# Kernel optimization log

Hardware: AMD Instinct MI355X
Metric: run time of the kernel (lower is better)

## Reference

```python
import jax, jax.numpy as jnp
import numpy as np

N, E = 50000, 800000
IN_DIM = 128
OUT_DIM = 128
H = 8
D = OUT_DIM // H  # head_dim = 16
LN_EPS = 1e-5


def setup_inputs() -> dict:
    key = jax.random.key(0)
    ks = jax.random.split(key, 16)
    s_in = 1.0 / np.sqrt(IN_DIM)
    s_out = 1.0 / np.sqrt(OUT_DIM)
    return {
        "x": jax.random.normal(ks[0], (N, IN_DIM), dtype=jnp.float32),
        "edge_index": jax.random.randint(ks[1], (2, E), 0, N, dtype=jnp.int32),
        "edge_attr": jax.random.uniform(ks[2], (E,), dtype=jnp.float32),
        # per-head TransformerConv params, stacked over heads (heads=1 per conv)
        "Wq": jax.random.normal(ks[3], (H, IN_DIM, D), dtype=jnp.float32) * s_in,
        "bq": jnp.zeros((H, D), dtype=jnp.float32),
        "Wk": jax.random.normal(ks[4], (H, IN_DIM, D), dtype=jnp.float32) * s_in,
        "bk": jnp.zeros((H, D), dtype=jnp.float32),
        "Wv": jax.random.normal(ks[5], (H, IN_DIM, D), dtype=jnp.float32) * s_in,
        "bv": jnp.zeros((H, D), dtype=jnp.float32),
        "We": jax.random.normal(ks[6], (H, D), dtype=jnp.float32),  # lin_edge (edge_dim=1, no bias)
        "Wskip": jax.random.normal(ks[7], (H, IN_DIM, D), dtype=jnp.float32) * s_in,
        "bskip": jnp.zeros((H, D), dtype=jnp.float32),
        "Wo": jax.random.normal(ks[8], (OUT_DIM, OUT_DIM), dtype=jnp.float32) * s_out,
        "bo": jnp.zeros((OUT_DIM,), dtype=jnp.float32),
        "gamma": jnp.ones((OUT_DIM,), dtype=jnp.float32),
        "beta": jnp.zeros((OUT_DIM,), dtype=jnp.float32),
    }


def reference(x, edge_index, edge_attr, Wq, bq, Wk, bk, Wv, bv, We, Wskip, bskip, Wo, bo, gamma, beta):
    n = x.shape[0]
    h, _, d = Wq.shape
    src, dst = edge_index[0], edge_index[1]
    # node-level projections for all heads at once: [N, H, D]
    q = jnp.einsum('ni,hid->nhd', x, Wq) + bq
    k = jnp.einsum('ni,hid->nhd', x, Wk) + bk
    v = jnp.einsum('ni,hid->nhd', x, Wv) + bv
    # edge embedding: lin_edge on scalar edge_attr -> [E, H, D]
    e = edge_attr[:, None, None] * We[None, :, :]
    # attention logits per edge/head: q_dst . (k_src + e) / sqrt(d)
    ke = k[src] + e
    alpha = jnp.einsum('ehd,ehd->eh', q[dst], ke) / jnp.sqrt(jnp.asarray(d, x.dtype))
    # segment softmax over destination nodes
    m = jax.ops.segment_max(alpha, dst, num_segments=n)  # [N, H]
    m = jnp.where(jnp.isfinite(m), m, 0.0)
    ex = jnp.exp(alpha - m[dst])
    denom = jax.ops.segment_sum(ex, dst, num_segments=n)
    w = ex / jnp.maximum(denom[dst], 1e-16)  # [E, H]
    # weighted aggregation of (v_src + e)
    agg = jax.ops.segment_sum(w[:, :, None] * (v[src] + e), dst, num_segments=n)  # [N, H, D]
    # root/skip connection inside each TransformerConv
    skip = jnp.einsum('ni,hid->nhd', x, Wskip) + bskip
    heads_cat = (agg + skip).reshape(n, h * d)  # concat over heads -> [N, OUT_DIM]
    out = heads_cat @ Wo + bo
    out = out + x  # residual (in_dim == out_dim)
    mu = out.mean(-1, keepdims=True)
    var = out.var(-1, keepdims=True)
    out = (out - mu) * jax.lax.rsqrt(var + LN_EPS) * gamma + beta
    return out
```

## Files before the change

### kernel.cpp

```cpp
#include <hip/hip_runtime.h>
#include <stdint.h>
#include <math.h>

#define IN_DIM 128
#define H_HEADS 8
#define HD 16

typedef __attribute__((ext_vector_type(8))) short bf16x8;
typedef __attribute__((ext_vector_type(4))) float f32x4;

__device__ __forceinline__ unsigned short f2bf_rne(float f) {
    unsigned int u = __float_as_uint(f);
    unsigned int r = (u + 0x7fffu + ((u >> 16) & 1u)) >> 16;
    return (unsigned short)r;
}
__device__ __forceinline__ float bf2f(unsigned short h) {
    return __uint_as_float(((unsigned int)h) << 16);
}

__device__ __forceinline__ void split_f8(const float4 f0, const float4 f1,
                                         bf16x8& h8, bf16x8& l8) {
    float ff[8] = {f0.x, f0.y, f0.z, f0.w, f1.x, f1.y, f1.z, f1.w};
    union { bf16x8 v; unsigned short u[8]; } H, L;
#pragma unroll
    for (int j = 0; j < 8; ++j) {
        H.u[j] = f2bf_rne(ff[j]);
        L.u[j] = f2bf_rne(ff[j] - bf2f(H.u[j]));
    }
    h8 = H.v; l8 = L.v;
}

__device__ __forceinline__ void stage_B(const unsigned short* __restrict__ src,
                                        unsigned short* __restrict__ lds, int t)
{
#pragma unroll
    for (int j = 0; j < 8; ++j) {
        int idx16 = t + j * 256;
        int c = idx16 >> 4, kcol = idx16 & 15;
        uint4 v = *reinterpret_cast<const uint4*>(src + (size_t)c * 128 + kcol * 8);
        *reinterpret_cast<uint4*>(lds + c * 128 + ((kcol ^ (c & 15)) * 8)) = v;
    }
}
__device__ __forceinline__ bf16x8 read_B(const unsigned short* __restrict__ lds,
                                         int c, int kcol)
{
    return *reinterpret_cast<const bf16x8*>(lds + c * 128 + ((kcol ^ (c & 15)) * 8));
}

__global__ __launch_bounds__(256)
void prep_count_kernel(const float* __restrict__ Wq, const float* __restrict__ Wk,
                       const float* __restrict__ Wv, const float* __restrict__ Wsk,
                       const float* __restrict__ Wo,
                       const float* __restrict__ bq, const float* __restrict__ bk,
                       const float* __restrict__ bv, const float* __restrict__ bsk,
                       unsigned short* __restrict__ WtH, unsigned short* __restrict__ WtL,
                       float* __restrict__ bias_cat,
                       const int* __restrict__ ei, int* __restrict__ deg, int E)
{
    const int b = blockIdx.x;
    const int t = threadIdx.x;
    if (b >= 5) {
        int e = (b - 5) * 256 + t;
        if (e < E) atomicAdd(&deg[ei[E + e]], 1);
        return;
    }
    const int p = b;
    const float* src = (p == 0) ? Wq : (p == 1) ? Wk : (p == 2) ? Wv : (p == 3) ? Wsk : Wo;
    unsigned short* dh = WtH + (size_t)p * 16384;
    unsigned short* dl = WtL + (size_t)p * 16384;
#pragma unroll
    for (int j = 0; j < 64; ++j) {
        int o = t + j * 256;
        int c = o >> 7, k = o & 127;
        float v;
        if (p < 4) {
            int h = c >> 4, d = c & 15;
            v = src[(size_t)h * 2048 + (size_t)k * 16 + d];
        } else {
            v = src[(size_t)k * 128 + c];
        }
        unsigned short hi = f2bf_rne(v);
        unsigned short lo = f2bf_rne(v - bf2f(hi));
        dh[o] = hi; dl[o] = lo;
    }
    if (p < 4 && t < 128) {
        const float* bb = (p == 0) ? bq : (p == 1) ? bk : (p == 2) ? bv : bsk;
        bias_cat[p * 128 + t] = bb[t];
    }
}

__global__ __launch_bounds__(256)
void gemm_proj_kernel(const float* __restrict__ A,
                      const unsigned short* __restrict__ WtH_base,
                      const unsigned short* __restrict__ WtL_base,
                      const float* __restrict__ bias_cat,
                      float* __restrict__ qout, float* __restrict__ skipout,
                      unsigned short* __restrict__ kvout, int N)
{
    __shared__ unsigned short Bs[16384];
    const int t = threadIdx.x;
    const int lane = t & 63;
    const int w = t >> 6;
    const int lr = lane & 15;
    const int lk = lane >> 4;
    const int p = blockIdx.y;
    const int brow0 = blockIdx.x * 64 + w * 16;
    const int arow = min(brow0 + lr, N - 1);
    const float* ap = A + (size_t)arow * 128;

    bf16x8 ah[4], al[4];
#pragma unroll
    for (int ks = 0; ks < 4; ++ks) {
        float4 f0 = *reinterpret_cast<const float4*>(ap + ks * 32 + lk * 8);
        float4 f1 = *reinterpret_cast<const float4*>(ap + ks * 32 + lk * 8 + 4);
        split_f8(f0, f1, ah[ks], al[ks]);
    }

    f32x4 acc[8];
#pragma unroll
    for (int ni = 0; ni < 8; ++ni) acc[ni] = (f32x4){0.f, 0.f, 0.f, 0.f};

    stage_B(WtH_base + (size_t)p * 16384, Bs, t);
    __syncthreads();
#pragma unroll
    for (int ks = 0; ks < 4; ++ks)
#pragma unroll
        for (int ni = 0; ni < 8; ++ni) {
            bf16x8 bh = read_B(Bs, ni * 16 + lr, ks * 4 + lk);
            acc[ni] = __builtin_amdgcn_mfma_f32_16x16x32_bf16(ah[ks], bh, acc[ni], 0, 0, 0);
            acc[ni] = __builtin_amdgcn_mfma_f32_16x16x32_bf16(al[ks], bh, acc[ni], 0, 0, 0);
        }
    __syncthreads();
    stage_B(WtL_base + (size_t)p * 16384, Bs, t);
    __syncthreads();
#pragma unroll
    for (int ks = 0; ks < 4; ++ks)
#pragma unroll
        for (int ni = 0; ni < 8; ++ni) {
            bf16x8 bl = read_B(Bs, ni * 16 + lr, ks * 4 + lk);
            acc[ni] = __builtin_amdgcn_mfma_f32_16x16x32_bf16(ah[ks], bl, acc[ni], 0, 0, 0);
        }

    const float* bias = bias_cat + p * 128;
    if (p == 0 || p == 3) {
        float* outp = (p == 0) ? qout : skipout;
#pragma unroll
        for (int ni = 0; ni < 8; ++ni) {
            int col = ni * 16 + lr;
            float bc = bias[col];
#pragma unroll
            for (int r = 0; r < 4; ++r) {
                int gr = brow0 + lk * 4 + r;
                if (gr < N) outp[(size_t)gr * 128 + col] = acc[ni][r] + bc;
            }
        }
    } else {
        unsigned int* kvu = (unsigned int*)kvout;
        const int slot = (p == 1) ? 0 : 1;
#pragma unroll
        for (int ni = 0; ni < 8; ++ni) {
            int col = ni * 16 + lr;
            float bc = bias[col];
#pragma unroll
            for (int r = 0; r < 4; ++r) {
                unsigned int s = f2bf_rne(acc[ni][r] + bc);
                unsigned int o = __shfl_xor((int)s, 1);
                int gr = brow0 + lk * 4 + r;
                if (((lr & 1) == 0) && gr < N)
                    kvu[(size_t)gr * 128 + 2 * (col >> 1) + slot] = s | (o << 16);
            }
        }
    }
}

__global__ __launch_bounds__(256)
void gemm_out_ln_kernel(const float* __restrict__ A,
                        const unsigned short* __restrict__ BtH_t,
                        const unsigned short* __restrict__ BtL_t,
                        const float* __restrict__ bo,
                        const float* __restrict__ res,
                        const float* __restrict__ gamma,
                        const float* __restrict__ beta,
                        float* __restrict__ out, int N)
{
    __shared__ unsigned short Bs[16384];
    __shared__ float lnS[2][32], lnSq[2][32];
    const int t = threadIdx.x;
    const int lane = t & 63;
    const int w = t >> 6;
    const int lr = lane & 15;
    const int lk = lane >> 4;
    const int ch = w & 1;
    const int rg = w >> 1;
    const int brow0 = blockIdx.x * 32 + rg * 16;
    const int arow = min(brow0 + lr, N - 1);
    const float* ap = A + (size_t)arow * 128;

    bf16x8 ah[4], al[4];
#pragma unroll
    for (int ks = 0; ks < 4; ++ks) {
        float4 f0 = *reinterpret_cast<const float4*>(ap + ks * 32 + lk * 8);
        float4 f1 = *reinterpret_cast<const float4*>(ap + ks * 32 + lk * 8 + 4);
        split_f8(f0, f1, ah[ks], al[ks]);
    }

    f32x4 acc[4];
#pragma unroll
    for (int ni = 0; ni < 4; ++ni) acc[ni] = (f32x4){0.f, 0.f, 0.f, 0.f};

    stage_B(BtH_t, Bs, t);
    __syncthreads();
#pragma unroll
    for (int ks = 0; ks < 4; ++ks)
#pragma unroll
        for (int ni = 0; ni < 4; ++ni) {
            bf16x8 bh = read_B(Bs, ch * 64 + ni * 16 + lr, ks * 4 + lk);
            acc[ni] = __builtin_amdgcn_mfma_f32_16x16x32_bf16(ah[ks], bh, acc[ni], 0, 0, 0);
            acc[ni] = __builtin_amdgcn_mfma_f32_16x16x32_bf16(al[ks], bh, acc[ni], 0, 0, 0);
        }
    __syncthreads();
    stage_B(BtL_t, Bs, t);
    __syncthreads();
#pragma unroll
    for (int ks = 0; ks < 4; ++ks)
#pragma unroll
        for (int ni = 0; ni < 4; ++ni) {
            bf16x8 bl = read_B(Bs, ch * 64 + ni * 16 + lr, ks * 4 + lk);
            acc[ni] = __builtin_amdgcn_mfma_f32_16x16x32_bf16(ah[ks], bl, acc[ni], 0, 0, 0);
        }

#pragma unroll
    for (int ni = 0; ni < 4; ++ni) {
        int col = ch * 64 + ni * 16 + lr;
        float bc = bo[col];
#pragma unroll
        for (int r = 0; r < 4; ++r) {
            int gr = brow0 + lk * 4 + r;
            float rv = (gr < N) ? res[(size_t)gr * 128 + col] : 0.f;
            acc[ni][r] += bc + rv;
        }
    }
    float ps[4], pq[4];
#pragma unroll
    for (int r = 0; r < 4; ++r) {
        float s = 0.f, sq = 0.f;
#pragma unroll
        for (int ni = 0; ni < 4; ++ni) { float v = acc[ni][r]; s += v; sq += v * v; }
#pragma unroll
        for (int mk = 1; mk < 16; mk <<= 1) {
            s  += __shfl_xor(s, mk);
            sq += __shfl_xor(sq, mk);
        }
        ps[r] = s; pq[r] = sq;
    }
    if (lr == 0) {
#pragma unroll
        for (int r = 0; r < 4; ++r) {
            lnS [ch][rg * 16 + lk * 4 + r] = ps[r];
            lnSq[ch][rg * 16 + lk * 4 + r] = pq[r];
        }
    }
    __syncthreads();
#pragma unroll
    for (int r = 0; r < 4; ++r) {
        int rib = rg * 16 + lk * 4 + r;
        float s  = lnS [0][rib] + lnS [1][rib];
        float sq = lnSq[0][rib] + lnSq[1][rib];
        float mean = s * (1.0f / 128.0f);
        float var  = sq * (1.0f / 128.0f) - mean * mean;
        float inv  = rsqrtf(var + 1e-5f);
        int gr = brow0 + lk * 4 + r;
        if (gr < N) {
#pragma unroll
            for (int ni = 0; ni < 4; ++ni) {
                int col = ch * 64 + ni * 16 + lr;
                out[(size_t)gr * 128 + col] =
                    (acc[ni][r] - mean) * inv * gamma[col] + beta[col];
            }
        }
    }
}

__global__ __launch_bounds__(1024)
void scan_kernel(const int* __restrict__ deg, int* __restrict__ offs,
                 int* __restrict__ cursor, int N)
{
    __shared__ int wsum[16];
    __shared__ int chunk_total_s;
    const int t = threadIdx.x;
    const int lane = t & 63, wid = t >> 6;
    int running = 0;
    for (int base = 0; base < N; base += 4096) {
        int v[4];
        int idx = base + t * 4;
#pragma unroll
        for (int j = 0; j < 4; ++j) { int i = idx + j; v[j] = (i < N) ? deg[i] : 0; }
        int ls = v[0] + v[1] + v[2] + v[3];
        int inc = ls;
#pragma unroll
        for (int off = 1; off < 64; off <<= 1) {
            int y = __shfl_up(inc, off);
            if (lane >= off) inc += y;
        }
        if (lane == 63) wsum[wid] = inc;
        __syncthreads();
        if (t < 16) {
            int winc = wsum[t];
            for (int off = 1; off < 16; off <<= 1) {
                int y = __shfl_up(winc, off);
                if (t >= off) winc += y;
            }
            wsum[t] = winc;
            if (t == 15) chunk_total_s = winc;
        }
        __syncthreads();
        int wexcl = (wid == 0) ? 0 : wsum[wid - 1];
        int texcl = running + wexcl + (inc - ls);
        int pre = 0;
#pragma unroll
        for (int j = 0; j < 4; ++j) {
            int i = idx + j;
            if (i < N) { offs[i] = texcl + pre; cursor[i] = texcl + pre; }
            pre += v[j];
        }
        running += chunk_total_s;
        __syncthreads();
    }
    if (t == 0) offs[N] = running;
}

__global__ void scatter_kernel(const int* __restrict__ ei, const float* __restrict__ ea,
                               int* __restrict__ cursor, int2* __restrict__ csr, int E)
{
    int e = blockIdx.x * 256 + threadIdx.x;
    if (e < E) {
        int s = ei[e], d = ei[E + e];
        int pos = atomicAdd(&cursor[d], 1);
        csr[pos] = make_int2(s, __float_as_int(ea[e]));
    }
}

#define GATHER(ec) (*reinterpret_cast<const ushort4*>(kvb + (size_t)(ec).x * 256 + 4 * lane))
#define PROCESS(ec, g, m, s, a0, a1) do { \
    float eav_ = __int_as_float((ec).y); \
    float ew0_ = eav_ * we2.x, ew1_ = eav_ * we2.y; \
    float dot_ = q2.x * (bf2f((g).x) + ew0_) + q2.y * (bf2f((g).y) + ew1_); \
    dot_ += __shfl_xor(dot_, 1); \
    dot_ += __shfl_xor(dot_, 2); \
    dot_ += __shfl_xor(dot_, 4); \
    float alpha_ = dot_ * 0.25f; \
    float d_ = alpha_ - (m); \
    float e_ = __expf(-fabsf(d_)); \
    bool up_ = d_ > 0.f; \
    float pv_ = up_ ? 1.f : e_; \
    float sc_ = up_ ? e_ : 1.f; \
    (m) = up_ ? alpha_ : (m); \
    (s) = (s) * sc_ + pv_; \
    (a0) = (a0) * sc_ + pv_ * (bf2f((g).z) + ew0_); \
    (a1) = (a1) * sc_ + pv_ * (bf2f((g).w) + ew1_); \
} while (0)

__global__ __launch_bounds__(256)
void agg_kernel(const float* __restrict__ qb, const float* __restrict__ sb,
                const unsigned short* __restrict__ kvb,
                const int* __restrict__ offs, const int2* __restrict__ csr,
                const float* __restrict__ We, float* __restrict__ heads_cat, int N)
{
    const int lane = threadIdx.x & 63;
    const int node = blockIdx.x * 4 + (threadIdx.x >> 6);
    if (node >= N) return;

    const float2 q2  = *reinterpret_cast<const float2*>(qb + (size_t)node * 128 + 2 * lane);
    const float2 we2 = *reinterpret_cast<const float2*>(We + 2 * lane);

    const int e0 = offs[node];
    const int cnt = offs[node + 1] - e0;

    float mA = -__builtin_huge_valf(), sA = 0.f, a0A = 0.f, a1A = 0.f;
    float mB = -__builtin_huge_valf(), sB = 0.f, a0B = 0.f, a1B = 0.f;

    int2 c0, c1, c2, c3, c4, c5;
    ushort4 g0, g1, g2, g3;
    if (cnt > 0) c0 = csr[e0];
    if (cnt > 1) c1 = csr[e0 + 1];
    if (cnt > 2) c2 = csr[e0 + 2];
    if (cnt > 3) c3 = csr[e0 + 3];
    if (cnt > 4) c4 = csr[e0 + 4];
    if (cnt > 5) c5 = csr[e0 + 5];
    if (cnt > 0) g0 = GATHER(c0);
    if (cnt > 1) g1 = GATHER(c1);
    if (cnt > 2) g2 = GATHER(c2);
    if (cnt > 3) g3 = GATHER(c3);

    int i = 0;
    for (; i + 1 < cnt; i += 2) {
        PROCESS(c0, g0, mA, sA, a0A, a1A);
        PROCESS(c1, g1, mB, sB, a0B, a1B);
        c0 = c2; c1 = c3; g0 = g2; g1 = g3;
        c2 = c4; c3 = c5;
        if (i + 6 < cnt) c4 = csr[e0 + i + 6];
        if (i + 7 < cnt) c5 = csr[e0 + i + 7];
        if (i + 4 < cnt) g2 = GATHER(c2);
        if (i + 5 < cnt) g3 = GATHER(c3);
    }
    if (i < cnt) PROCESS(c0, g0, mA, sA, a0A, a1A);

    float s, a0, a1;
    {
        float nm = fmaxf(mA, mB);
        float eA = (cnt > 0) ? __expf(mA - nm) : 0.f;
        float eB = (cnt > 1) ? __expf(mB - nm) : 0.f;
        s  = sA * eA + sB * eB;
        a0 = a0A * eA + a0B * eB;
        a1 = a1A * eA + a1B * eB;
    }

    float inv = 1.0f / fmaxf(s, 1e-16f);
    const float2 sk = *reinterpret_cast<const float2*>(sb + (size_t)node * 128 + 2 * lane);
    float2 o;
    o.x = a0 * inv + sk.x;
    o.y = a1 * inv + sk.y;
    *reinterpret_cast<float2*>(heads_cat + (size_t)node * 128 + 2 * lane) = o;
}

extern "C" void kernel_launch(void* const* d_in, const int* in_sizes, int n_in,
                              void* d_out, int out_size, void* d_ws, size_t ws_size,
                              hipStream_t stream)
{
    const float* x    = (const float*)d_in[0];
    const int*   ei   = (const int*)d_in[1];
    const float* ea   = (const float*)d_in[2];
    const float* Wq   = (const float*)d_in[3];
    const float* bq   = (const float*)d_in[4];
    const float* Wk   = (const float*)d_in[5];
    const float* bk   = (const float*)d_in[6];
    const float* Wv   = (const float*)d_in[7];
    const float* bv   = (const float*)d_in[8];
    const float* We   = (const float*)d_in[9];
    const float* Wsk  = (const float*)d_in[10];
    const float* bsk  = (const float*)d_in[11];
    const float* Wo   = (const float*)d_in[12];
    const float* bo   = (const float*)d_in[13];
    const float* gamma= (const float*)d_in[14];
    const float* beta = (const float*)d_in[15];
    const int N = in_sizes[0] / 128;
    const int E = in_sizes[1] / 2;
    float* out = (float*)d_out;

    char* w = (char*)d_ws;
    float* qarr      = (float*)w; w += (size_t)N * 128 * sizeof(float);
    float* skiparr   = (float*)w; w += (size_t)N * 128 * sizeof(float);
    unsigned short* kv = (unsigned short*)w; w += (size_t)N * 256 * sizeof(unsigned short);
    float* heads_cat = (float*)w; w += (size_t)N * 128 * sizeof(float);
    int*   deg       = (int*)w;   w += ((size_t)N + 16) * sizeof(int);
    int*   offs      = (int*)w;   w += ((size_t)N + 16) * sizeof(int);
    int*   cursor    = (int*)w;   w += ((size_t)N + 16) * sizeof(int);
    int2*  csr       = (int2*)w;  w += (size_t)E * sizeof(int2);
    unsigned short* WtH = (unsigned short*)w; w += (size_t)5 * 16384 * sizeof(unsigned short);
    unsigned short* WtL = (unsigned short*)w; w += (size_t)5 * 16384 * sizeof(unsigned short);
    float* bias_cat  = (float*)w; w += 4 * 128 * sizeof(float);

    hipMemsetAsync(deg, 0, (size_t)N * sizeof(int), stream);

    const int cntBlocks = (E + 255) / 256;
    prep_count_kernel<<<5 + cntBlocks, 256, 0, stream>>>(Wq, Wk, Wv, Wsk, Wo, bq, bk, bv, bsk,
                                                         WtH, WtL, bias_cat, ei, deg, E);

    dim3 gProj((N + 63) / 64, 4);
    gemm_proj_kernel<<<gProj, 256, 0, stream>>>(x, WtH, WtL, bias_cat, qarr, skiparr, kv, N);

    scan_kernel<<<1, 1024, 0, stream>>>(deg, offs, cursor, N);
    scatter_kernel<<<(E + 255) / 256, 256, 0, stream>>>(ei, ea, cursor, csr, E);
    agg_kernel<<<(N + 3) / 4, 256, 0, stream>>>(qarr, skiparr, kv, offs, csr, We, heads_cat, N);

    gemm_out_ln_kernel<<<(N + 31) / 32, 256, 0, stream>>>(heads_cat,
                                                          WtH + (size_t)4 * 16384,
                                                          WtL + (size_t)4 * 16384,
                                                          bo, x, gamma, beta, out, N);
}
```

Measured before the change: 376.5 us.

## Split each node's edges across two half-waves with 16-byte KV gathers

The aggregation kernel now has each half of a 64-lane wave handle alternate edges of a node. Each lane covers 4 channels with a single 16-byte load of interleaved K/V bf16, and the two partial online-softmax states are merged with cross-half shuffles. The edge-embedding term in the logit is precomputed once per node as q·We, so each edge needs fewer shuffle steps and multiplies. The bf16 conversion helper is also swapped for the HIP intrinsic. The aim is more independent gathers in flight and fewer per-edge reductions, at the cost of more registers and an extra merge step per node.

Measured after the change: 357.0 us. 1.05x faster.

```diff
diff --git a/kernel.cpp b/kernel.cpp
--- a/kernel.cpp
+++ b/kernel.cpp
@@ -1,4 +1,5 @@
 #include <hip/hip_runtime.h>
+#include <hip/hip_bf16.h>
 #include <stdint.h>
 #include <math.h>
 
@@ -9,10 +10,9 @@
 typedef __attribute__((ext_vector_type(8))) short bf16x8;
 typedef __attribute__((ext_vector_type(4))) float f32x4;
 
-__device__ __forceinline__ unsigned short f2bf_rne(float f) {
-    unsigned int u = __float_as_uint(f);
-    unsigned int r = (u + 0x7fffu + ((u >> 16) & 1u)) >> 16;
-    return (unsigned short)r;
+__device__ __forceinline__ unsigned short f2bf(float f) {
+    __hip_bfloat16 h = __float2bfloat16(f);
+    return reinterpret_cast<unsigned short&>(h);
 }
 __device__ __forceinline__ float bf2f(unsigned short h) {
     return __uint_as_float(((unsigned int)h) << 16);
@@ -24,8 +24,8 @@
     union { bf16x8 v; unsigned short u[8]; } H, L;
 #pragma unroll
     for (int j = 0; j < 8; ++j) {
-        H.u[j] = f2bf_rne(ff[j]);
-        L.u[j] = f2bf_rne(ff[j] - bf2f(H.u[j]));
+        H.u[j] = f2bf(ff[j]);
+        L.u[j] = f2bf(ff[j] - bf2f(H.u[j]));
     }
     h8 = H.v; l8 = L.v;
 }
@@ -79,8 +79,8 @@
         } else {
             v = src[(size_t)k * 128 + c];
         }
-        unsigned short hi = f2bf_rne(v);
-        unsigned short lo = f2bf_rne(v - bf2f(hi));
+        unsigned short hi = f2bf(v);
+        unsigned short lo = f2bf(v - bf2f(hi));
         dh[o] = hi; dl[o] = lo;
     }
     if (p < 4 && t < 128) {
@@ -163,7 +163,7 @@
             float bc = bias[col];
 #pragma unroll
             for (int r = 0; r < 4; ++r) {
-                unsigned int s = f2bf_rne(acc[ni][r] + bc);
+                unsigned int s = f2bf(acc[ni][r] + bc);
                 unsigned int o = __shfl_xor((int)s, 1);
                 int gr = brow0 + lk * 4 + r;
                 if (((lr & 1) == 0) && gr < N)
@@ -340,26 +340,6 @@
     }
 }
 
-#define GATHER(ec) (*reinterpret_cast<const ushort4*>(kvb + (size_t)(ec).x * 256 + 4 * lane))
-#define PROCESS(ec, g, m, s, a0, a1) do { \
-    float eav_ = __int_as_float((ec).y); \
-    float ew0_ = eav_ * we2.x, ew1_ = eav_ * we2.y; \
-    float dot_ = q2.x * (bf2f((g).x) + ew0_) + q2.y * (bf2f((g).y) + ew1_); \
-    dot_ += __shfl_xor(dot_, 1); \
-    dot_ += __shfl_xor(dot_, 2); \
-    dot_ += __shfl_xor(dot_, 4); \
-    float alpha_ = dot_ * 0.25f; \
-    float d_ = alpha_ - (m); \
-    float e_ = __expf(-fabsf(d_)); \
-    bool up_ = d_ > 0.f; \
-    float pv_ = up_ ? 1.f : e_; \
-    float sc_ = up_ ? e_ : 1.f; \
-    (m) = up_ ? alpha_ : (m); \
-    (s) = (s) * sc_ + pv_; \
-    (a0) = (a0) * sc_ + pv_ * (bf2f((g).z) + ew0_); \
-    (a1) = (a1) * sc_ + pv_ * (bf2f((g).w) + ew1_); \
-} while (0)
-
 __global__ __launch_bounds__(256)
 void agg_kernel(const float* __restrict__ qb, const float* __restrict__ sb,
                 const unsigned short* __restrict__ kvb,
@@ -369,58 +349,94 @@
     const int lane = threadIdx.x & 63;
     const int node = blockIdx.x * 4 + (threadIdx.x >> 6);
     if (node >= N) return;
-
-    const float2 q2  = *reinterpret_cast<const float2*>(qb + (size_t)node * 128 + 2 * lane);
-    const float2 we2 = *reinterpret_cast<const float2*>(We + 2 * lane);
+    const int h32 = lane & 31;
+    const int half = lane >> 5;
+
+    const float4 q4  = *reinterpret_cast<const float4*>(qb + (size_t)node * 128 + 4 * h32);
+    const float4 we4 = *reinterpret_cast<const float4*>(We + 4 * h32);
+
+    float qwe = q4.x * we4.x + q4.y * we4.y + q4.z * we4.z + q4.w * we4.w;
+    qwe += __shfl_xor(qwe, 1);
+    qwe += __shfl_xor(qwe, 2);
 
     const int e0 = offs[node];
     const int cnt = offs[node + 1] - e0;
-
-    float mA = -__builtin_huge_valf(), sA = 0.f, a0A = 0.f, a1A = 0.f;
-    float mB = -__builtin_huge_valf(), sB = 0.f, a0B = 0.f, a1B = 0.f;
-
-    int2 c0, c1, c2, c3, c4, c5;
-    ushort4 g0, g1, g2, g3;
-    if (cnt > 0) c0 = csr[e0];
-    if (cnt > 1) c1 = csr[e0 + 1];
-    if (cnt > 2) c2 = csr[e0 + 2];
-    if (cnt > 3) c3 = csr[e0 + 3];
-    if (cnt > 4) c4 = csr[e0 + 4];
-    if (cnt > 5) c5 = csr[e0 + 5];
-    if (cnt > 0) g0 = GATHER(c0);
-    if (cnt > 1) g1 = GATHER(c1);
-    if (cnt > 2) g2 = GATHER(c2);
-    if (cnt > 3) g3 = GATHER(c3);
-
-    int i = 0;
-    for (; i + 1 < cnt; i += 2) {
-        PROCESS(c0, g0, mA, sA, a0A, a1A);
-        PROCESS(c1, g1, mB, sB, a0B, a1B);
-        c0 = c2; c1 = c3; g0 = g2; g1 = g3;
-        c2 = c4; c3 = c5;
-        if (i + 6 < cnt) c4 = csr[e0 + i + 6];
-        if (i + 7 < cnt) c5 = csr[e0 + i + 7];
-        if (i + 4 < cnt) g2 = GATHER(c2);
-        if (i + 5 < cnt) g3 = GATHER(c3);
-    }
-    if (i < cnt) PROCESS(c0, g0, mA, sA, a0A, a1A);
-
-    float s, a0, a1;
-    {
-        float nm = fmaxf(mA, mB);
-        float eA = (cnt > 0) ? __expf(mA - nm) : 0.f;
-        float eB = (cnt > 1) ? __expf(mB - nm) : 0.f;
-        s  = sA * eA + sB * eB;
-        a0 = a0A * eA + a0B * eB;
-        a1 = a1A * eA + a1B * eB;
-    }
-
-    float inv = 1.0f / fmaxf(s, 1e-16f);
-    const float2 sk = *reinterpret_cast<const float2*>(sb + (size_t)node * 128 + 2 * lane);
-    float2 o;
-    o.x = a0 * inv + sk.x;
-    o.y = a1 * inv + sk.y;
-    *reinterpret_cast<float2*>(heads_cat + (size_t)node * 128 + 2 * lane) = o;
+    const int myCnt = (cnt > half) ? ((cnt - half + 1) >> 1) : 0;
+    const int2* cp = csr + e0 + half;
+
+    float m = -__builtin_huge_valf();
+    float s = 0.f, a0 = 0.f, a1 = 0.f, a2 = 0.f, a3 = 0.f;
+
+#define KVG(ec) (*reinterpret_cast<const uint4*>(kvb + (size_t)(ec).x * 256 + 8 * h32))
+#define PROC(ec, u) do { \
+    float eav_ = __int_as_float((ec).y); \
+    float k0_ = __uint_as_float((u).x << 16); \
+    float k1_ = __uint_as_float((u).x & 0xffff0000u); \
+    float k2_ = __uint_as_float((u).z << 16); \
+    float k3_ = __uint_as_float((u).z & 0xffff0000u); \
+    float part_ = q4.x * k0_ + q4.y * k1_ + q4.z * k2_ + q4.w * k3_; \
+    part_ += __shfl_xor(part_, 1); \
+    part_ += __shfl_xor(part_, 2); \
+    float alpha_ = (part_ + eav_ * qwe) * 0.25f; \
+    float d_ = alpha_ - m; \
+    float e_ = __expf(-fabsf(d_)); \
+    bool up_ = d_ > 0.f; \
+    float pv_ = up_ ? 1.f : e_; \
+    float sc_ = up_ ? e_ : 1.f; \
+    m = up_ ? alpha_ : m; \
+    float t_ = pv_ * eav_; \
+    float v0_ = __uint_as_float((u).y << 16); \
+    float v1_ = __uint_as_float((u).y & 0xffff0000u); \
+    float v2_ = __uint_as_float((u).w << 16); \
+    float v3_ = __uint_as_float((u).w & 0xffff0000u); \
+    s  = fmaf(s,  sc_, pv_); \
+    a0 = fmaf(a0, sc_, fmaf(t_, we4.x, pv_ * v0_)); \
+    a1 = fmaf(a1, sc_, fmaf(t_, we4.y, pv_ * v1_)); \
+    a2 = fmaf(a2, sc_, fmaf(t_, we4.z, pv_ * v2_)); \
+    a3 = fmaf(a3, sc_, fmaf(t_, we4.w, pv_ * v3_)); \
+} while (0)
+
+    int2 c0v, c1v, cnv;
+    uint4 g0v, g1v;
+    if (myCnt > 0) c0v = cp[0];
+    if (myCnt > 1) c1v = cp[2];
+    if (myCnt > 0) g0v = KVG(c0v);
+    if (myCnt > 1) g1v = KVG(c1v);
+
+    for (int j = 0; j < myCnt; ++j) {
+        if (j + 2 < myCnt) cnv = cp[2 * j + 4];
+        PROC(c0v, g0v);
+        c0v = c1v; g0v = g1v; c1v = cnv;
+        if (j + 2 < myCnt) g1v = KVG(c1v);
+    }
+
+    float om = __shfl_xor(m, 32);
+    float os = __shfl_xor(s, 32);
+    float o0 = __shfl_xor(a0, 32);
+    float o1 = __shfl_xor(a1, 32);
+    float o2 = __shfl_xor(a2, 32);
+    float o3 = __shfl_xor(a3, 32);
+    float nm = fmaxf(m, om);
+    float eS = (s  > 0.f) ? __expf(m  - nm) : 0.f;
+    float eO = (os > 0.f) ? __expf(om - nm) : 0.f;
+    float st = s * eS + os * eO;
+    float r0 = a0 * eS + o0 * eO;
+    float r1 = a1 * eS + o1 * eO;
+    float r2 = a2 * eS + o2 * eO;
+    float r3 = a3 * eS + o3 * eO;
+
+    if (half == 0) {
+        float inv = 1.0f / fmaxf(st, 1e-16f);
+        const float4 sk = *reinterpret_cast<const float4*>(sb + (size_t)node * 128 + 4 * h32);
+        float4 o;
+        o.x = r0 * inv + sk.x;
+        o.y = r1 * inv + sk.y;
+        o.z = r2 * inv + sk.z;
+        o.w = r3 * inv + sk.w;
+        *reinterpret_cast<float4*>(heads_cat + (size_t)node * 128 + 4 * h32) = o;
+    }
+#undef KVG
+#undef PROC
 }
 
 extern "C" void kernel_launch(void* const* d_in, const int* in_sizes, int n_in,
```
